# Kernel optimization log

Measured on AMD Instinct MI355X. Metric: run time of the kernel, lower is better.

## Reference

```python
import jax, jax.numpy as jnp
import numpy as np

B, N, NODE_DIM = 32, 512, 2
D, H, L, FF = 512, 8, 3, 2048
DK = D // H  # key/val dim per head = 64
EPS = 1e-5


def batch_norm(h, gamma, beta):
    # BatchNorm1d in training mode over flattened (batch*graph) dim, biased var
    flat = h.reshape(-1, h.shape[-1])
    mu = flat.mean(axis=0)
    var = flat.var(axis=0)
    out = (flat - mu) * jax.lax.rsqrt(var + EPS) * gamma + beta
    return out.reshape(h.shape)


def mha(h, Wq, Wk, Wv, Wo):
    # h: [B,N,D]; Wq/Wk/Wv: [H,D,DK]; Wo: [H,DK,D]
    Q = jnp.einsum('bnd,hdk->hbnk', h, Wq)
    K = jnp.einsum('bnd,hdk->hbnk', h, Wk)
    V = jnp.einsum('bnd,hdk->hbnk', h, Wv)
    scores = jnp.einsum('hbqk,hbnk->hbqn', Q, K) / jnp.sqrt(jnp.float32(DK))
    attn = jax.nn.softmax(scores, axis=-1)
    heads = jnp.einsum('hbqn,hbnk->hbqk', attn, V)
    return jnp.einsum('hbqk,hkd->bqd', heads, Wo)


def setup_inputs() -> dict:
    key = jax.random.key(0)
    ks = jax.random.split(key, 16)
    u = lambda k, shape, fan: jax.random.uniform(k, shape, jnp.float32, -1.0, 1.0) / np.sqrt(fan)
    return {
        'x': jax.random.normal(ks[0], (B, N, NODE_DIM), jnp.float32),
        'We': u(ks[1], (D, NODE_DIM), NODE_DIM),
        'be': u(ks[2], (D,), NODE_DIM),
        'Wq': u(ks[3], (L, H, D, DK), DK),
        'Wk': u(ks[4], (L, H, D, DK), DK),
        'Wv': u(ks[5], (L, H, D, DK), DK),
        'Wo': u(ks[6], (L, H, DK, D), D),
        'g1': jnp.ones((L, D), jnp.float32),
        'b1': jnp.zeros((L, D), jnp.float32),
        'W1': u(ks[7], (L, FF, D), D),
        'bb1': u(ks[8], (L, FF), D),
        'W2': u(ks[9], (L, D, FF), FF),
        'bb2': u(ks[10], (L, D), FF),
        'g2': jnp.ones((L, D), jnp.float32),
        'b2': jnp.zeros((L, D), jnp.float32),
    }


def reference(x, We, be, Wq, Wk, Wv, Wo, g1, b1, W1, bb1, W2, bb2, g2, b2):
    # init embed: Linear(node_dim -> D)
    h = jnp.einsum('bnc,dc->bnd', x, We) + be
    for i in range(L):
        h = batch_norm(h + mha(h, Wq[i], Wk[i], Wv[i], Wo[i]), g1[i], b1[i])
        ff = jax.nn.relu(jnp.einsum('bnd,fd->bnf', h, W1[i]) + bb1[i])
        ff = jnp.einsum('bnf,df->bnd', ff, W2[i]) + bb2[i]
        h = batch_norm(h + ff, g2[i], b2[i])
    return h, h.mean(axis=1)
```

## Files before the change

kernel.cpp:

```cpp
#include <hip/hip_runtime.h>
#include <hip/hip_bf16.h>

#define Bx 32
#define Nx 512
#define Dx 512
#define Hx 8
#define DKx 64
#define FFx 2048
#define TOK (Bx * Nx)
#define EPSx 1e-5f

typedef float  f32x4  __attribute__((ext_vector_type(4)));
typedef _Float16 hfrag8 __attribute__((ext_vector_type(8)));
typedef _Float16 h4     __attribute__((ext_vector_type(4)));

struct hf2 { _Float16 hi, lo; };
__device__ __forceinline__ hf2 split2h(float v) {
    _Float16 h = (_Float16)v;
    hf2 r; r.hi = h; r.lo = (_Float16)(v - (float)h);
    return r;
}

__device__ __forceinline__ void gl16(const void* g, void* l) {
    __builtin_amdgcn_global_load_lds(
        (const __attribute__((address_space(1))) unsigned int*)g,
        (__attribute__((address_space(3))) unsigned int*)l, 16, 0, 0);
}

__device__ __forceinline__ int swzoff(int row, int q) {
    int p = row >> 1;
    int sl = ((row & 1) << 2) | q;
    int s = sl ^ (p & 7);
    return p * 128 + s * 16;
}

__device__ __forceinline__ float ldsel(const void* p32, const void* p16, size_t i, int f32) {
    return f32 ? ((const float*)p32)[i]
               : __bfloat162float(((const __hip_bfloat16*)p16)[i]);
}

__global__ void detect_kernel(const void* __restrict__ x, int* __restrict__ flag)
{
    if (threadIdx.x == 0 && blockIdx.x == 0) {
        const unsigned short* u = (const unsigned short*)x;
        int hits = 0;
        for (int i = 0; i < 256; ++i) {
            int e = (u[i] >> 7) & 0xFF;
            if (e >= 0x86) ++hits;
        }
        *flag = (hits > 8) ? 1 : 0;
    }
}

__global__ __launch_bounds__(256) void cvt_kernel(
    const void* __restrict__ W, _Float16* __restrict__ o, const int* __restrict__ dtp)
{
    const int f32 = *dtp;
    size_t idx = (size_t)blockIdx.x * 256 + threadIdx.x;
    o[idx] = (_Float16)ldsel(W, W, idx, f32);
}

__global__ __launch_bounds__(256) void transpose_cvt_kernel(
    const void* __restrict__ W, _Float16* __restrict__ o,
    int R, int C, const int* __restrict__ dtp)
{
    const int f32 = *dtp;
    __shared__ float tile[64][65];
    const size_t mbase = (size_t)blockIdx.z * R * C;
    const int c0 = blockIdx.x * 64, r0 = blockIdx.y * 64;
    const int tc = threadIdx.x & 63, tg = threadIdx.x >> 6;
    #pragma unroll
    for (int i = 0; i < 16; ++i) {
        int r = tg * 16 + i;
        tile[r][tc] = ldsel(W, W, mbase + (size_t)(r0 + r) * C + c0 + tc, f32);
    }
    __syncthreads();
    #pragma unroll
    for (int i = 0; i < 16; ++i) {
        int cc = tg * 16 + i;
        o[mbase + (size_t)(c0 + cc) * R + r0 + tc] = (_Float16)tile[tc][cc];
    }
}

__global__ __launch_bounds__(256) void embed_kernel(
    const void* __restrict__ x, const void* __restrict__ We,
    const void* __restrict__ be, _Float16* __restrict__ hh, _Float16* __restrict__ hl,
    const int* __restrict__ dtp)
{
    const int f32 = *dtp;
    size_t idx = (size_t)blockIdx.x * 256 + threadIdx.x;
    int d = idx & (Dx - 1);
    size_t t = idx >> 9;
    float v = ldsel(x, x, t * 2, f32)     * ldsel(We, We, d * 2, f32) +
              ldsel(x, x, t * 2 + 1, f32) * ldsel(We, We, d * 2 + 1, f32) +
              ldsel(be, be, d, f32);
    hf2 s = split2h(v);
    hh[idx] = s.hi; hl[idx] = s.lo;
}

template <int NMF, int EPI, int OHF>
__global__ __launch_bounds__(256, NMF == 2 ? 3 : 4) void gemm3(
    const _Float16* __restrict__ Ahg, const _Float16* __restrict__ Alg,
    const _Float16* __restrict__ Bg,
    const void* __restrict__ bias32, const void* __restrict__ bias16,
    const _Float16* __restrict__ residH, const _Float16* __restrict__ residL,
    void* __restrict__ outp, int M, int N, int K, const int* __restrict__ dtp)
{
    constexpr int PLANES = NMF + 1;
    constexpr int BUFB = PLANES * 8192;
    constexpr int BOFF = NMF * 8192;
    const int f32 = *dtp;
    __shared__ __align__(16) unsigned char lds[2][BUFB];

    const int tid = threadIdx.x;
    const int gx = gridDim.x;
    const int nwg = gx * gridDim.y;
    int flat = blockIdx.y * gx + blockIdx.x;
    flat = (flat & 7) * (nwg >> 3) + (flat >> 3);
    const int bm = (flat / gx) * 128;
    const int bn = (flat % gx) * 128;

    const int lane = tid & 63, wv = tid >> 6;
    const int quad = lane >> 4, lrow = lane & 15;
    const int wm = (wv & 1) * 64, wn = (wv >> 1) * 64;

    f32x4 acc[4][4] = {};

    const int s2 = (lane & 7) ^ (lane >> 3);
    const int rl = 2 * (lane >> 3) + (s2 >> 2);
    const int cl = (s2 & 3) * 8;

    const _Float16* wsrc;
    int wrb;
    bool doStage;
    if constexpr (NMF == 2) {
        doStage = (wv < 3);
        wsrc = (wv == 0) ? Ahg : (wv == 1) ? Alg : Bg;
        wrb  = (wv < 2) ? bm : bn;
    } else {
        doStage = (wv < 2);
        wsrc = (wv == 0) ? Ahg : Bg;
        wrb  = (wv == 0) ? bm : bn;
    }

    auto stage = [&](int buf, int k0) {
        if (doStage) {
            const _Float16* s = wsrc + (size_t)(wrb + rl) * K + k0 + cl;
            #pragma unroll
            for (int ch = 0; ch < 8; ++ch)
                gl16(s + (size_t)(ch * 16) * K, &lds[buf][wv * 8192 + ch * 1024]);
        }
    };

    int offA[4], offB[4];
    #pragma unroll
    for (int mt = 0; mt < 4; ++mt) offA[mt] = swzoff(wm + mt * 16 + lrow, quad);
    #pragma unroll
    for (int nt = 0; nt < 4; ++nt) offB[nt] = BOFF + swzoff(wn + nt * 16 + lrow, quad);

    stage(0, 0);
    if (32 < K) stage(1, 32);

    int cur = 0;
    for (int k0 = 0; k0 < K; k0 += 32) {
        if (k0 + 32 < K) asm volatile("s_waitcnt vmcnt(8)" ::: "memory");
        else             asm volatile("s_waitcnt vmcnt(0)" ::: "memory");
        __builtin_amdgcn_sched_barrier(0);
        __builtin_amdgcn_s_barrier();
        __builtin_amdgcn_sched_barrier(0);

        const unsigned char* bp = lds[cur];
        hfrag8 ah[4], alo[4];
        #pragma unroll
        for (int mt = 0; mt < 4; ++mt) {
            ah[mt] = *(const hfrag8*)(bp + offA[mt]);
            if constexpr (NMF == 2) alo[mt] = *(const hfrag8*)(bp + offA[mt] + 8192);
        }
        #pragma unroll
        for (int nt = 0; nt < 4; ++nt) {
            hfrag8 b = *(const hfrag8*)(bp + offB[nt]);
            #pragma unroll
            for (int mt = 0; mt < 4; ++mt) {
                acc[mt][nt] = __builtin_amdgcn_mfma_f32_16x16x32_f16(ah[mt], b, acc[mt][nt], 0, 0, 0);
                if constexpr (NMF == 2)
                    acc[mt][nt] = __builtin_amdgcn_mfma_f32_16x16x32_f16(alo[mt], b, acc[mt][nt], 0, 0, 0);
            }
        }

        __builtin_amdgcn_sched_barrier(0);
        asm volatile("s_waitcnt lgkmcnt(0)" ::: "memory");
        __builtin_amdgcn_s_barrier();
        __builtin_amdgcn_sched_barrier(0);

        if (k0 + 64 < K) stage(cur, k0 + 64);
        cur ^= 1;
    }

    #pragma unroll
    for (int mt = 0; mt < 4; ++mt)
        #pragma unroll
        for (int nt = 0; nt < 4; ++nt)
            #pragma unroll
            for (int reg = 0; reg < 4; ++reg) {
                int m = bm + wm + mt * 16 + quad * 4 + reg;
                int n = bn + wn + nt * 16 + lrow;
                float v = acc[mt][nt][reg];
                if constexpr (EPI == 1) { v += ldsel(bias32, bias16, n, f32); v = fmaxf(v, 0.f); }
                if constexpr (EPI == 2) {
                    if (bias32) v += ldsel(bias32, bias16, n, f32);
                    size_t ridx = (size_t)m * N + n;
                    v += (float)residH[ridx] + (float)residL[ridx];
                }
                if constexpr (OHF) ((_Float16*)outp)[(size_t)m * N + n] = (_Float16)v;
                else               ((float*)outp)[(size_t)m * N + n] = v;
            }
}

__global__ __launch_bounds__(256, 3) void qkv_mfma(
    const _Float16* __restrict__ Ahg, const _Float16* __restrict__ Alg,
    const _Float16* __restrict__ QT, const _Float16* __restrict__ KT,
    const _Float16* __restrict__ VT,
    _Float16* __restrict__ Qhg, _Float16* __restrict__ Qlg,
    _Float16* __restrict__ Khg, _Float16* __restrict__ Vo, int M, int K)
{
    __shared__ __align__(16) unsigned char lds[2][3 * 8192];

    const int tid = threadIdx.x;
    const int gx = gridDim.x;
    const int nwg = gx * gridDim.y;
    int flat = blockIdx.y * gx + blockIdx.x;
    flat = (flat & 7) * (nwg >> 3) + (flat >> 3);
    const int bm = (flat / gx) * 128;
    const int bn = (flat % gx) * 128;

    const int sel = bn >> 9;
    const int nloc = bn & 511;
    const _Float16* Bg = ((sel == 0) ? QT : (sel == 1) ? KT : VT) + (size_t)nloc * K;

    const int lane = tid & 63, wv = tid >> 6;
    const int quad = lane >> 4, lrow = lane & 15;
    const int wm = (wv & 1) * 64, wn = (wv >> 1) * 64;

    f32x4 acc[4][4] = {};

    const int s2 = (lane & 7) ^ (lane >> 3);
    const int rl = 2 * (lane >> 3) + (s2 >> 2);
    const int cl = (s2 & 3) * 8;

    const bool doStage = (wv < 3);
    const _Float16* wsrc = (wv == 0) ? Ahg : (wv == 1) ? Alg : Bg;
    const int wrb = (wv < 2) ? bm : 0;

    auto stage = [&](int buf, int k0) {
        if (doStage) {
            const _Float16* s = wsrc + (size_t)(wrb + rl) * K + k0 + cl;
            #pragma unroll
            for (int ch = 0; ch < 8; ++ch)
                gl16(s + (size_t)(ch * 16) * K, &lds[buf][wv * 8192 + ch * 1024]);
        }
    };

    int offA[4], offB[4];
    #pragma unroll
    for (int mt = 0; mt < 4; ++mt) offA[mt] = swzoff(wm + mt * 16 + lrow, quad);
    #pragma unroll
    for (int nt = 0; nt < 4; ++nt) offB[nt] = 16384 + swzoff(wn + nt * 16 + lrow, quad);

    stage(0, 0);
    if (32 < K) stage(1, 32);

    int cur = 0;
    for (int k0 = 0; k0 < K; k0 += 32) {
        if (k0 + 32 < K) asm volatile("s_waitcnt vmcnt(8)" ::: "memory");
        else             asm volatile("s_waitcnt vmcnt(0)" ::: "memory");
        __builtin_amdgcn_sched_barrier(0);
        __builtin_amdgcn_s_barrier();
        __builtin_amdgcn_sched_barrier(0);

        const unsigned char* bp = lds[cur];
        hfrag8 ah[4], alo[4];
        #pragma unroll
        for (int mt = 0; mt < 4; ++mt) {
            ah[mt]  = *(const hfrag8*)(bp + offA[mt]);
            alo[mt] = *(const hfrag8*)(bp + offA[mt] + 8192);
        }
        #pragma unroll
        for (int nt = 0; nt < 4; ++nt) {
            hfrag8 b = *(const hfrag8*)(bp + offB[nt]);
            #pragma unroll
            for (int mt = 0; mt < 4; ++mt) {
                acc[mt][nt] = __builtin_amdgcn_mfma_f32_16x16x32_f16(ah[mt],  b, acc[mt][nt], 0, 0, 0);
                acc[mt][nt] = __builtin_amdgcn_mfma_f32_16x16x32_f16(alo[mt], b, acc[mt][nt], 0, 0, 0);
            }
        }

        __builtin_amdgcn_sched_barrier(0);
        asm volatile("s_waitcnt lgkmcnt(0)" ::: "memory");
        __builtin_amdgcn_s_barrier();
        __builtin_amdgcn_sched_barrier(0);

        if (k0 + 64 < K) stage(cur, k0 + 64);
        cur ^= 1;
    }

    const int nb = M >> 9;
    #pragma unroll
    for (int mt = 0; mt < 4; ++mt)
        #pragma unroll
        for (int nt = 0; nt < 4; ++nt) {
            const int ncol = nloc + wn + nt * 16 + lrow;
            const int head = ncol >> 6, dk = ncol & 63;
            const int m0 = bm + wm + mt * 16 + quad * 4;
            const int b_ = m0 >> 9, q = m0 & 511;
            if (sel == 2) {
                h4 v;
                #pragma unroll
                for (int reg = 0; reg < 4; ++reg) v[reg] = (_Float16)acc[mt][nt][reg];
                *(h4*)&Vo[(((size_t)head * nb + b_) * DKx + dk) * Nx + q] = v;
            } else if (sel == 1) {
                #pragma unroll
                for (int reg = 0; reg < 4; ++reg) {
                    size_t oidx = (((size_t)head * nb + b_) * Nx + (q + reg)) * DKx + dk;
                    Khg[oidx] = (_Float16)acc[mt][nt][reg];
                }
            } else {
                #pragma unroll
                for (int reg = 0; reg < 4; ++reg) {
                    hf2 s = split2h(acc[mt][nt][reg]);
                    size_t oidx = (((size_t)head * nb + b_) * Nx + (q + reg)) * DKx + dk;
                    Qhg[oidx] = s.hi;
                    Qlg[oidx] = s.lo;
                }
            }
        }
}

__global__ __launch_bounds__(256, 4) void attn_kernel(
    const _Float16* __restrict__ Qhg, const _Float16* __restrict__ Qlg,
    const _Float16* __restrict__ Khg, const _Float16* __restrict__ Vtg,
    _Float16* __restrict__ headsH, _Float16* __restrict__ headsL)
{
    __shared__ __align__(16) _Float16  Kh[64][72];
    __shared__ __align__(16) _Float16  Vt[64][72];
    __shared__ __align__(16) _Float16  Sp[64][72];
    __shared__ float ml[64], ll[64], al[64];

    const int tid = threadIdx.x;
    const int q0 = blockIdx.x * 64;
    const int hb = blockIdx.y;
    const size_t base = (size_t)hb * (Nx * DKx);
    const int lane = tid & 63, wv = tid >> 6;
    const int quad = lane >> 4, lrow = lane & 15;
    const int wm = (wv & 1) * 32, wn = (wv >> 1) * 32;
    const int sr = tid >> 2, sc = (tid & 3) * 16;

    {
        size_t off = base + (size_t)(q0 + sr) * DKx + sc;
        *(hfrag8*)&Kh[sr][sc]     = *(const hfrag8*)(Qhg + off);
        *(hfrag8*)&Kh[sr][sc + 8] = *(const hfrag8*)(Qhg + off + 8);
        *(hfrag8*)&Sp[sr][sc]     = *(const hfrag8*)(Qlg + off);
        *(hfrag8*)&Sp[sr][sc + 8] = *(const hfrag8*)(Qlg + off + 8);
    }
    if (tid < 64) { ml[tid] = -INFINITY; ll[tid] = 0.f; }
    __syncthreads();

    hfrag8 qh[2][2], qlo[2][2];
    #pragma unroll
    for (int mt = 0; mt < 2; ++mt)
        #pragma unroll
        for (int ks = 0; ks < 2; ++ks) {
            qh[mt][ks]  = *(const hfrag8*)&Kh[wm + mt * 16 + lrow][ks * 32 + quad * 8];
            qlo[mt][ks] = *(const hfrag8*)&Sp[wm + mt * 16 + lrow][ks * 32 + quad * 8];
        }
    __syncthreads();

    hfrag8 pkh[2], pv[2];
    auto loadKV = [&](int n0) {
        size_t off = base + (size_t)(n0 + sr) * DKx + sc;
        pkh[0] = *(const hfrag8*)(Khg + off);
        pkh[1] = *(const hfrag8*)(Khg + off + 8);
        const _Float16* vp = Vtg + base + (size_t)sr * Nx + n0 + sc;
        pv[0] = *(const hfrag8*)vp;
        pv[1] = *(const hfrag8*)(vp + 8);
    };
    auto storeKV = [&]() {
        *(hfrag8*)&Kh[sr][sc]     = pkh[0];
        *(hfrag8*)&Kh[sr][sc + 8] = pkh[1];
        *(hfrag8*)&Vt[sr][sc]     = pv[0];
        *(hfrag8*)&Vt[sr][sc + 8] = pv[1];
    };

    f32x4 accO[2][2] = {};

    loadKV(0); storeKV();
    __syncthreads();

    for (int n0 = 0; n0 < Nx; n0 += 64) {
        const bool more = (n0 + 64 < Nx);
        if (more) loadKV(n0 + 64);

        f32x4 accS[2][2] = {};
        #pragma unroll
        for (int ks = 0; ks < 2; ++ks) {
            hfrag8 bh[2];
            #pragma unroll
            for (int nt = 0; nt < 2; ++nt)
                bh[nt] = *(const hfrag8*)&Kh[wn + nt * 16 + lrow][ks * 32 + quad * 8];
            #pragma unroll
            for (int mt = 0; mt < 2; ++mt)
                #pragma unroll
                for (int nt = 0; nt < 2; ++nt) {
                    accS[mt][nt] = __builtin_amdgcn_mfma_f32_16x16x32_f16(qh[mt][ks],  bh[nt], accS[mt][nt], 0, 0, 0);
                    accS[mt][nt] = __builtin_amdgcn_mfma_f32_16x16x32_f16(qlo[mt][ks], bh[nt], accS[mt][nt], 0, 0, 0);
                }
        }
        #pragma unroll
        for (int mt = 0; mt < 2; ++mt)
            #pragma unroll
            for (int nt = 0; nt < 2; ++nt)
                #pragma unroll
                for (int reg = 0; reg < 4; ++reg)
                    Sp[wm + mt * 16 + quad * 4 + reg][wn + nt * 16 + lrow] =
                        (_Float16)(accS[mt][nt][reg] * 0.125f);
        __syncthreads();

        {
            hfrag8 s0 = *(const hfrag8*)&Sp[sr][sc];
            hfrag8 s1 = *(const hfrag8*)&Sp[sr][sc + 8];
            float rmax = -INFINITY;
            #pragma unroll
            for (int j = 0; j < 8; ++j) {
                rmax = fmaxf(rmax, (float)s0[j]);
                rmax = fmaxf(rmax, (float)s1[j]);
            }
            rmax = fmaxf(rmax, __shfl_xor(rmax, 1));
            rmax = fmaxf(rmax, __shfl_xor(rmax, 2));
            float mold = ml[sr];
            float mnew = fmaxf(mold, rmax);
            float sum = 0.f;
            hfrag8 p0, p1;
            #pragma unroll
            for (int j = 0; j < 8; ++j) {
                float pa = __expf((float)s0[j] - mnew);
                float pb = __expf((float)s1[j] - mnew);
                sum += pa + pb;
                p0[j] = (_Float16)pa;
                p1[j] = (_Float16)pb;
            }
            sum += __shfl_xor(sum, 1);
            sum += __shfl_xor(sum, 2);
            *(hfrag8*)&Sp[sr][sc]     = p0;
            *(hfrag8*)&Sp[sr][sc + 8] = p1;
            if ((tid & 3) == 0) {
                float alpha = __expf(mold - mnew);
                ml[sr] = mnew;
                ll[sr] = ll[sr] * alpha + sum;
                al[sr] = alpha;
            }
        }
        __syncthreads();

        #pragma unroll
        for (int mt = 0; mt < 2; ++mt) {
            float a0 = al[wm + mt * 16 + quad * 4 + 0];
            float a1 = al[wm + mt * 16 + quad * 4 + 1];
            float a2 = al[wm + mt * 16 + quad * 4 + 2];
            float a3 = al[wm + mt * 16 + quad * 4 + 3];
            #pragma unroll
            for (int nt = 0; nt < 2; ++nt) {
                accO[mt][nt][0] *= a0; accO[mt][nt][1] *= a1;
                accO[mt][nt][2] *= a2; accO[mt][nt][3] *= a3;
            }
        }
        #pragma unroll
        for (int ks = 0; ks < 2; ++ks) {
            hfrag8 ap[2], bv[2];
            #pragma unroll
            for (int mt = 0; mt < 2; ++mt)
                ap[mt] = *(const hfrag8*)&Sp[wm + mt * 16 + lrow][ks * 32 + quad * 8];
            #pragma unroll
            for (int nt = 0; nt < 2; ++nt)
                bv[nt] = *(const hfrag8*)&Vt[wn + nt * 16 + lrow][ks * 32 + quad * 8];
            #pragma unroll
            for (int mt = 0; mt < 2; ++mt)
                #pragma unroll
                for (int nt = 0; nt < 2; ++nt)
                    accO[mt][nt] = __builtin_amdgcn_mfma_f32_16x16x32_f16(ap[mt], bv[nt], accO[mt][nt], 0, 0, 0);
        }

        if (more) {
            __syncthreads();
            storeKV();
            __syncthreads();
        }
    }

    const int h_ = hb >> 5, b_ = hb & 31;
    #pragma unroll
    for (int mt = 0; mt < 2; ++mt)
        #pragma unroll
        for (int reg = 0; reg < 4; ++reg) {
            int qrow = wm + mt * 16 + quad * 4 + reg;
            float invl = 1.f / ll[qrow];
            size_t tok = (size_t)b_ * Nx + (q0 + qrow);
            #pragma unroll
            for (int nt = 0; nt < 2; ++nt) {
                int dk = wn + nt * 16 + lrow;
                hf2 s = split2h(accO[mt][nt][reg] * invl);
                size_t oidx = tok * Dx + h_ * DKx + dk;
                headsH[oidx] = s.hi;
                headsL[oidx] = s.lo;
            }
        }
}

__global__ __launch_bounds__(256) void bn_stats(const float* __restrict__ t, float* __restrict__ stats)
{
    int r0 = blockIdx.x * 16;
    int c = threadIdx.x;
    float s0 = 0, q0 = 0, s1 = 0, q1 = 0;
    for (int r = 0; r < 16; ++r) {
        const float* row = t + (size_t)(r0 + r) * Dx;
        float v0 = row[c], v1 = row[c + 256];
        s0 += v0; q0 += v0 * v0; s1 += v1; q1 += v1 * v1;
    }
    atomicAdd(&stats[c], s0);
    atomicAdd(&stats[c + 256], s1);
    atomicAdd(&stats[Dx + c], q0);
    atomicAdd(&stats[Dx + c + 256], q1);
}

__global__ __launch_bounds__(256) void bn_norm(
    const float* __restrict__ t, const float* __restrict__ stats,
    const void* __restrict__ g32, const void* __restrict__ g16,
    const void* __restrict__ b32, const void* __restrict__ b16,
    _Float16* __restrict__ hh, _Float16* __restrict__ hl, const int* __restrict__ dtp)
{
    const int f32 = *dtp;
    size_t idx = (size_t)blockIdx.x * 256 + threadIdx.x;
    int c = idx & (Dx - 1);
    const float invM = 1.f / (float)TOK;
    float mu = stats[c] * invM;
    float var = stats[Dx + c] * invM - mu * mu;
    float v = (t[idx] - mu) * rsqrtf(var + EPSx) * ldsel(g32, g16, c, f32) + ldsel(b32, b16, c, f32);
    hf2 s = split2h(v);
    hh[idx] = s.hi; hl[idx] = s.lo;
}

__global__ __launch_bounds__(256) void out_h_kernel(
    const _Float16* __restrict__ hh, const _Float16* __restrict__ hl, float* __restrict__ out)
{
    size_t idx = (size_t)blockIdx.x * 256 + threadIdx.x;
    out[idx] = (float)hh[idx] + (float)hl[idx];
}

__global__ __launch_bounds__(256) void out_mean_part(
    const _Float16* __restrict__ hh, const _Float16* __restrict__ hl, float* __restrict__ part)
{
    int b = blockIdx.x;
    int g = blockIdx.y;
    int d = threadIdx.x;
    float s0 = 0.f, s1 = 0.f;
    for (int n = g * 64; n < g * 64 + 64; ++n) {
        size_t idx = ((size_t)b * Nx + n) * Dx;
        s0 += (float)hh[idx + d]       + (float)hl[idx + d];
        s1 += (float)hh[idx + d + 256] + (float)hl[idx + d + 256];
    }
    part[((size_t)b * 8 + g) * Dx + d]       = s0;
    part[((size_t)b * 8 + g) * Dx + d + 256] = s1;
}

__global__ __launch_bounds__(256) void out_mean_final(
    const float* __restrict__ part, float* __restrict__ out2)
{
    size_t o = (size_t)blockIdx.x * 256 + threadIdx.x;
    int b = (int)(o >> 9), d = (int)(o & 511);
    float s = 0.f;
    #pragma unroll
    for (int g = 0; g < 8; ++g) s += part[((size_t)b * 8 + g) * Dx + d];
    out2[o] = s * (1.f / (float)Nx);
}

extern "C" void kernel_launch(void* const* d_in, const int* in_sizes, int n_in,
                              void* d_out, int out_size, void* d_ws, size_t ws_size,
                              hipStream_t stream)
{
    const void* x   = d_in[0];
    const void* We  = d_in[1];
    const void* be  = d_in[2];
    const void* Wq  = d_in[3];
    const void* Wk  = d_in[4];
    const void* Wv  = d_in[5];
    const void* Wo  = d_in[6];
    const void* g1  = d_in[7];
    const void* b1  = d_in[8];
    const void* W1  = d_in[9];
    const void* bb1 = d_in[10];
    const void* W2  = d_in[11];
    const void* bb2 = d_in[12];
    const void* g2  = d_in[13];
    const void* b2  = d_in[14];

    const size_t szHD = (size_t)TOK * Dx;
    const size_t QKN  = (size_t)Hx * Bx * Nx * DKx;
    const size_t szQT = (size_t)3 * Hx * DKx * Dx;
    const size_t szW1 = (size_t)3 * FFx * Dx;
    const size_t szWqkvL = (size_t)Hx * Dx * DKx;

    float* t     = (float*)d_ws;
    float* stats = t + szHD;
    int*   dtp   = (int*)(stats + 2 * Dx);
    _Float16* hh = (_Float16*)(stats + 2 * Dx + 64);
    _Float16* hl = hh + szHD;
    _Float16* region = hl + szHD;

    _Float16* headsH = region;
    _Float16* headsL = headsH + szHD;
    _Float16* Qhg    = headsL + szHD;
    _Float16* Qlg    = Qhg + QKN;
    _Float16* Khg    = Qlg + QKN;
    _Float16* Vtg    = Khg + QKN;
    _Float16* ffbuf = region;

    _Float16* WqT = Vtg + QKN;
    _Float16* WkT = WqT + szQT;
    _Float16* WvT = WkT + szQT;
    _Float16* WoT = WvT + szQT;
    _Float16* W1c = WoT + szQT;
    _Float16* W2c = W1c + szW1;
    float*    part = (float*)(W2c + szW1);

    auto p32 = [](const void* p, size_t e) { return (const void*)((const float*)p + e); };
    auto p16 = [](const void* p, size_t e) { return (const void*)((const __hip_bfloat16*)p + e); };

    detect_kernel<<<1, 64, 0, stream>>>(x, dtp);

    transpose_cvt_kernel<<<dim3(1, 8, 24), 256, 0, stream>>>(Wq, WqT, Dx, DKx, dtp);
    transpose_cvt_kernel<<<dim3(1, 8, 24), 256, 0, stream>>>(Wk, WkT, Dx, DKx, dtp);
    transpose_cvt_kernel<<<dim3(1, 8, 24), 256, 0, stream>>>(Wv, WvT, Dx, DKx, dtp);
    transpose_cvt_kernel<<<dim3(8, 8, 3), 256, 0, stream>>>(Wo, WoT, Dx, Dx, dtp);
    cvt_kernel<<<szW1 / 256, 256, 0, stream>>>(W1, W1c, dtp);
    cvt_kernel<<<szW1 / 256, 256, 0, stream>>>(W2, W2c, dtp);

    embed_kernel<<<TOK * Dx / 256, 256, 0, stream>>>(x, We, be, hh, hl, dtp);

    const dim3 gQKV(12, TOK / 128);
    const dim3 gWo(Dx / 128, TOK / 128);
    const dim3 gAttn(Nx / 64, Hx * Bx);
    const dim3 gFF1(FFx / 128, TOK / 128);
    const dim3 gFF2(Dx / 128, TOK / 128);
    for (int l = 0; l < 3; ++l) {
        const size_t eQ = (size_t)l * szWqkvL;
        const size_t e1 = (size_t)l * FFx * Dx;
        const size_t eD = (size_t)l * Dx, eF = (size_t)l * FFx;

        qkv_mfma<<<gQKV, 256, 0, stream>>>(
            hh, hl, WqT + eQ, WkT + eQ, WvT + eQ,
            Qhg, Qlg, Khg, Vtg, TOK, Dx);
        attn_kernel<<<gAttn, 256, 0, stream>>>(Qhg, Qlg, Khg, Vtg, headsH, headsL);

        gemm3<2, 2, 0><<<gWo, 256, 0, stream>>>(
            headsH, headsL, WoT + eQ,
            nullptr, nullptr, hh, hl, t, TOK, Dx, Dx, dtp);

        hipMemsetAsync(stats, 0, 2 * Dx * sizeof(float), stream);
        bn_stats<<<1024, 256, 0, stream>>>(t, stats);
        bn_norm<<<TOK * Dx / 256, 256, 0, stream>>>(
            t, stats, p32(g1, eD), p16(g1, eD), p32(b1, eD), p16(b1, eD), hh, hl, dtp);

        gemm3<2, 1, 1><<<gFF1, 256, 0, stream>>>(
            hh, hl, W1c + e1,
            p32(bb1, eF), p16(bb1, eF), nullptr, nullptr, ffbuf, TOK, FFx, Dx, dtp);
        gemm3<1, 2, 0><<<gFF2, 256, 0, stream>>>(
            ffbuf, nullptr, W2c + e1,
            p32(bb2, eD), p16(bb2, eD), hh, hl, t, TOK, Dx, FFx, dtp);

        hipMemsetAsync(stats, 0, 2 * Dx * sizeof(float), stream);
        bn_stats<<<1024, 256, 0, stream>>>(t, stats);
        bn_norm<<<TOK * Dx / 256, 256, 0, stream>>>(
            t, stats, p32(g2, eD), p16(g2, eD), p32(b2, eD), p16(b2, eD), hh, hl, dtp);
    }

    out_h_kernel<<<TOK * Dx / 256, 256, 0, stream>>>(hh, hl, (float*)d_out);
    out_mean_part<<<dim3(Bx, 8), 256, 0, stream>>>(hh, hl, part);
    out_mean_final<<<Bx * Dx / 256, 256, 0, stream>>>(part, (float*)d_out + (size_t)TOK * Dx);
}
```

Baseline: 1.374 ms.

## Fuse batchnorm statistics into GEMM epilogue and raise MFMA wave priority

```diff
diff --git a/kernel.cpp b/kernel.cpp
--- a/kernel.cpp
+++ b/kernel.cpp
@@ -98,13 +98,14 @@
     hh[idx] = s.hi; hl[idx] = s.lo;
 }
 
-template <int NMF, int EPI, int OHF>
+template <int NMF, int EPI, int OHF, int STATS>
 __global__ __launch_bounds__(256, NMF == 2 ? 3 : 4) void gemm3(
     const _Float16* __restrict__ Ahg, const _Float16* __restrict__ Alg,
     const _Float16* __restrict__ Bg,
     const void* __restrict__ bias32, const void* __restrict__ bias16,
     const _Float16* __restrict__ residH, const _Float16* __restrict__ residL,
-    void* __restrict__ outp, int M, int N, int K, const int* __restrict__ dtp)
+    void* __restrict__ outp, float* __restrict__ part,
+    int M, int N, int K, const int* __restrict__ dtp)
 {
     constexpr int PLANES = NMF + 1;
     constexpr int BUFB = PLANES * 8192;
@@ -169,6 +170,7 @@
         __builtin_amdgcn_s_barrier();
         __builtin_amdgcn_sched_barrier(0);
 
+        __builtin_amdgcn_s_setprio(1);
         const unsigned char* bp = lds[cur];
         hfrag8 ah[4], alo[4];
         #pragma unroll
@@ -186,6 +188,7 @@
                     acc[mt][nt] = __builtin_amdgcn_mfma_f32_16x16x32_f16(alo[mt], b, acc[mt][nt], 0, 0, 0);
             }
         }
+        __builtin_amdgcn_s_setprio(0);
 
         __builtin_amdgcn_sched_barrier(0);
         asm volatile("s_waitcnt lgkmcnt(0)" ::: "memory");
@@ -197,13 +200,14 @@
     }
 
     #pragma unroll
-    for (int mt = 0; mt < 4; ++mt)
-        #pragma unroll
-        for (int nt = 0; nt < 4; ++nt)
+    for (int nt = 0; nt < 4; ++nt) {
+        const int n = bn + wn + nt * 16 + lrow;
+        float cs = 0.f, cq = 0.f;
+        #pragma unroll
+        for (int mt = 0; mt < 4; ++mt)
             #pragma unroll
             for (int reg = 0; reg < 4; ++reg) {
                 int m = bm + wm + mt * 16 + quad * 4 + reg;
-                int n = bn + wn + nt * 16 + lrow;
                 float v = acc[mt][nt][reg];
                 if constexpr (EPI == 1) { v += ldsel(bias32, bias16, n, f32); v = fmaxf(v, 0.f); }
                 if constexpr (EPI == 2) {
@@ -213,7 +217,18 @@
                 }
                 if constexpr (OHF) ((_Float16*)outp)[(size_t)m * N + n] = (_Float16)v;
                 else               ((float*)outp)[(size_t)m * N + n] = v;
-            }
+                if constexpr (STATS) { cs += v; cq += v * v; }
+            }
+        if constexpr (STATS) {
+            cs += __shfl_xor(cs, 16); cs += __shfl_xor(cs, 32);
+            cq += __shfl_xor(cq, 16); cq += __shfl_xor(cq, 32);
+            if (quad == 0) {
+                float* pb = part + (size_t)(bm >> 7) * 1024;
+                atomicAdd(&pb[n], cs);
+                atomicAdd(&pb[512 + n], cq);
+            }
+        }
+    }
 }
 
 __global__ __launch_bounds__(256, 3) void qkv_mfma(
@@ -277,6 +292,7 @@
         __builtin_amdgcn_s_barrier();
         __builtin_amdgcn_sched_barrier(0);
 
+        __builtin_amdgcn_s_setprio(1);
         const unsigned char* bp = lds[cur];
         hfrag8 ah[4], alo[4];
         #pragma unroll
@@ -293,6 +309,7 @@
                 acc[mt][nt] = __builtin_amdgcn_mfma_f32_16x16x32_f16(alo[mt], b, acc[mt][nt], 0, 0, 0);
             }
         }
+        __builtin_amdgcn_s_setprio(0);
 
         __builtin_amdgcn_sched_barrier(0);
         asm volatile("s_waitcnt lgkmcnt(0)" ::: "memory");
@@ -400,6 +417,7 @@
         if (more) loadKV(n0 + 64);
 
         f32x4 accS[2][2] = {};
+        __builtin_amdgcn_s_setprio(1);
         #pragma unroll
         for (int ks = 0; ks < 2; ++ks) {
             hfrag8 bh[2];
@@ -414,6 +432,7 @@
                     accS[mt][nt] = __builtin_amdgcn_mfma_f32_16x16x32_f16(qlo[mt][ks], bh[nt], accS[mt][nt], 0, 0, 0);
                 }
         }
+        __builtin_amdgcn_s_setprio(0);
         #pragma unroll
         for (int mt = 0; mt < 2; ++mt)
             #pragma unroll
@@ -472,6 +491,7 @@
                 accO[mt][nt][2] *= a2; accO[mt][nt][3] *= a3;
             }
         }
+        __builtin_amdgcn_s_setprio(1);
         #pragma unroll
         for (int ks = 0; ks < 2; ++ks) {
             hfrag8 ap[2], bv[2];
@@ -487,6 +507,7 @@
                 for (int nt = 0; nt < 2; ++nt)
                     accO[mt][nt] = __builtin_amdgcn_mfma_f32_16x16x32_f16(ap[mt], bv[nt], accO[mt][nt], 0, 0, 0);
         }
+        __builtin_amdgcn_s_setprio(0);
 
         if (more) {
             __syncthreads();
@@ -514,20 +535,13 @@
         }
 }
 
-__global__ __launch_bounds__(256) void bn_stats(const float* __restrict__ t, float* __restrict__ stats)
-{
-    int r0 = blockIdx.x * 16;
-    int c = threadIdx.x;
-    float s0 = 0, q0 = 0, s1 = 0, q1 = 0;
-    for (int r = 0; r < 16; ++r) {
-        const float* row = t + (size_t)(r0 + r) * Dx;
-        float v0 = row[c], v1 = row[c + 256];
-        s0 += v0; q0 += v0 * v0; s1 += v1; q1 += v1 * v1;
-    }
-    atomicAdd(&stats[c], s0);
-    atomicAdd(&stats[c + 256], s1);
-    atomicAdd(&stats[Dx + c], q0);
-    atomicAdd(&stats[Dx + c + 256], q1);
+__global__ __launch_bounds__(256) void bn_final(
+    const float* __restrict__ part, float* __restrict__ stats)
+{
+    int c = blockIdx.x * 256 + threadIdx.x;
+    float s = 0.f;
+    for (int rt = 0; rt < 128; ++rt) s += part[(size_t)rt * 1024 + c];
+    stats[c] = s;
 }
 
 __global__ __launch_bounds__(256) void bn_norm(
@@ -649,6 +663,7 @@
     const dim3 gAttn(Nx / 64, Hx * Bx);
     const dim3 gFF1(FFx / 128, TOK / 128);
     const dim3 gFF2(Dx / 128, TOK / 128);
+    const size_t partBytes = 128 * 1024 * sizeof(float);
     for (int l = 0; l < 3; ++l) {
         const size_t eQ = (size_t)l * szWqkvL;
         const size_t e1 = (size_t)l * FFx * Dx;
@@ -659,24 +674,22 @@
             Qhg, Qlg, Khg, Vtg, TOK, Dx);
         attn_kernel<<<gAttn, 256, 0, stream>>>(Qhg, Qlg, Khg, Vtg, headsH, headsL);
 
-        gemm3<2, 2, 0><<<gWo, 256, 0, stream>>>(
+        hipMemsetAsync(part, 0, partBytes, stream);
+        gemm3<2, 2, 0, 1><<<gWo, 256, 0, stream>>>(
             headsH, headsL, WoT + eQ,
-            nullptr, nullptr, hh, hl, t, TOK, Dx, Dx, dtp);
-
-        hipMemsetAsync(stats, 0, 2 * Dx * sizeof(float), stream);
-        bn_stats<<<1024, 256, 0, stream>>>(t, stats);
+            nullptr, nullptr, hh, hl, t, part, TOK, Dx, Dx, dtp);
+        bn_final<<<4, 256, 0, stream>>>(part, stats);
         bn_norm<<<TOK * Dx / 256, 256, 0, stream>>>(
             t, stats, p32(g1, eD), p16(g1, eD), p32(b1, eD), p16(b1, eD), hh, hl, dtp);
 
-        gemm3<2, 1, 1><<<gFF1, 256, 0, stream>>>(
+        gemm3<2, 1, 1, 0><<<gFF1, 256, 0, stream>>>(
             hh, hl, W1c + e1,
-            p32(bb1, eF), p16(bb1, eF), nullptr, nullptr, ffbuf, TOK, FFx, Dx, dtp);
-        gemm3<1, 2, 0><<<gFF2, 256, 0, stream>>>(
+            p32(bb1, eF), p16(bb1, eF), nullptr, nullptr, ffbuf, nullptr, TOK, FFx, Dx, dtp);
+        hipMemsetAsync(part, 0, partBytes, stream);
+        gemm3<1, 2, 0, 1><<<gFF2, 256, 0, stream>>>(
             ffbuf, nullptr, W2c + e1,
-            p32(bb2, eD), p16(bb2, eD), hh, hl, t, TOK, Dx, FFx, dtp);
-
-        hipMemsetAsync(stats, 0, 2 * Dx * sizeof(float), stream);
-        bn_stats<<<1024, 256, 0, stream>>>(t, stats);
+            p32(bb2, eD), p16(bb2, eD), hh, hl, t, part, TOK, Dx, FFx, dtp);
+        bn_final<<<4, 256, 0, stream>>>(part, stats);
         bn_norm<<<TOK * Dx / 256, 256, 0, stream>>>(
             t, stats, p32(g2, eD), p16(g2, eD), p32(b2, eD), p16(b2, eD), hh, hl, dtp);
     }
```

Result: no change. 1.381 ms (+0.5%).
